# Optimization experiments

Measured on AMD Instinct MI355X. Metric: run time of the kernel, lower is better.

Reference implementation:

```python
import jax, jax.numpy as jnp
import numpy as np

NUM_HEADS = 12


def setup_inputs() -> dict:
    key = jax.random.key(0)
    k1, k2, k3 = jax.random.split(key, 3)
    B, F, P, D = 8, 16, 196, 768
    x = jax.random.normal(k1, (B, F, P, D), dtype=jnp.float32)
    w_qkv = jax.random.normal(k2, (3 * D, D), dtype=jnp.float32) * (D ** -0.5)
    w_proj = jax.random.normal(k3, (D, D), dtype=jnp.float32) * (D ** -0.5)
    b_proj = jnp.zeros((D,), dtype=jnp.float32)
    return {"x": x, "w_qkv": w_qkv, "w_proj": w_proj, "b_proj": b_proj}


def reference(x, w_qkv, w_proj, b_proj):
    B, F, P, D = x.shape
    H = NUM_HEADS
    hd = D // H
    H2 = H // 2
    scale = hd ** -0.5
    N = F * P

    xf = x.reshape(B, N, D)
    qkv = jnp.einsum('bnd,ed->bne', xf, w_qkv)              # (B, N, 3D)
    qkv = qkv.reshape(B, N, 3, H, hd).transpose(2, 0, 3, 1, 4)
    q, k, v = qkv[0], qkv[1], qkv[2]                         # (B, H, N, hd)

    # split heads: first half spatial, second half temporal
    qs, qt = q[:, :H2], q[:, H2:]
    ks, kt = k[:, :H2], k[:, H2:]
    vs, vt = v[:, :H2], v[:, H2:]

    # spatial attention over patches within each frame
    qs = qs.reshape(B * F, H2, P, hd)
    ks = ks.reshape(B * F, H2, P, hd)
    vs = vs.reshape(B * F, H2, P, hd)
    attn_s = jax.nn.softmax(jnp.einsum('nhqd,nhkd->nhqk', qs, ks) * scale, axis=-1)
    ws = jnp.einsum('nhqk,nhkd->nhqd', attn_s, vs)           # (B*F, H2, P, hd)

    # temporal attention: raw row-major reshape, faithful to torch .reshape
    qt = qt.reshape(B * P, H2, F, hd)
    kt = kt.reshape(B * P, H2, F, hd)
    vt = vt.reshape(B * P, H2, F, hd)
    attn_t = jax.nn.softmax(jnp.einsum('mhqd,mhkd->mhqk', qt, kt) * scale, axis=-1)
    wt = jnp.einsum('mhqk,mhkd->mhqd', attn_t, vt)           # (B*P, H2, F, hd)

    ws = ws.reshape(B, H2, N, hd)
    wt = wt.reshape(B, H2, N, hd)
    w = jnp.concatenate([ws, wt], axis=1)                    # (B, H, N, hd)
    w = w.transpose(0, 2, 1, 3).reshape(B, N, D)

    out = jnp.einsum('bnd,ed->bne', w, w_proj) + b_proj
    return out.reshape(B, F, P, D)
```

## Files before the change

### kernel.cpp

```cpp
#include <hip/hip_runtime.h>

#define DEV __device__ __forceinline__

typedef _Float16 half8  __attribute__((ext_vector_type(8)));
typedef _Float16 half4h __attribute__((ext_vector_type(4)));
typedef float    f32x4  __attribute__((ext_vector_type(4)));

static constexpr int Bb = 8;
static constexpr int Ff = 16;
static constexpr int Pp = 196;
static constexpr int Dd = 768;
static constexpr int Hh = 12;
static constexpr int HD = 64;
static constexpr int Nn = 3136;
static constexpr int NC = 392;

#define MFMA(a, b, c) __builtin_amdgcn_mfma_f32_16x16x32_f16(a, b, c, 0, 0, 0)

DEV void gll16(const _Float16* g, _Float16* l) {
  __builtin_amdgcn_global_load_lds(
      (__attribute__((address_space(1))) void*)(g),
      (__attribute__((address_space(3))) void*)(l), 16, 0, 0);
}

DEV void lds_fence() { asm volatile("s_waitcnt lgkmcnt(0)" ::: "memory"); }

__global__ __launch_bounds__(256) void cvt_all(const float* __restrict__ x,
                                               const float* __restrict__ wq,
                                               const float* __restrict__ wp,
                                               _Float16* __restrict__ xh,
                                               _Float16* __restrict__ wqh,
                                               _Float16* __restrict__ wph) {
  const int NX = 4816896, NQ = 442368;
  int i = blockIdx.x * 256 + threadIdx.x;
  const float* s;
  _Float16* d;
  int j;
  if (i < NX) { s = x; d = xh; j = i; }
  else if (i < NX + NQ) { s = wq; d = wqh; j = i - NX; }
  else { s = wp; d = wph; j = i - NX - NQ; }
  f32x4 v = ((const f32x4*)s)[j];
  half4h h;
  h.x = (_Float16)v.x; h.y = (_Float16)v.y;
  h.z = (_Float16)v.z; h.w = (_Float16)v.w;
  ((half4h*)d)[j] = h;
}

__global__ __launch_bounds__(256) void gemm_qkv(const _Float16* __restrict__ X,
                                                const _Float16* __restrict__ W,
                                                _Float16* __restrict__ Q8,
                                                _Float16* __restrict__ K8,
                                                _Float16* __restrict__ V8) {
  __shared__ __align__(16) _Float16 smem[128 * 132];
  _Float16* As = smem;
  _Float16* Bs = smem + 128 * 32;
  const int tid = threadIdx.x;
  const int lane = tid & 63, wid = tid >> 6;
  const int l15 = lane & 15, quad = lane >> 4;
  const int L = blockIdx.x;
  const int v = (L & 7) * 441 + (L >> 3);
  const int bx = v % 18, by = v / 18;
  const int row0 = by * 128;
  const int e0 = bx * 128;
  const int wm = (wid >> 1) * 64, wn = (wid & 1) * 64;

  const _Float16* Ag = X + (size_t)row0 * Dd;
  const _Float16* Bg = W + (size_t)e0 * Dd;

  f32x4 acc[4][4];
#pragma unroll
  for (int i = 0; i < 4; ++i)
#pragma unroll
    for (int j = 0; j < 4; ++j) acc[i][j] = (f32x4)0.0f;

  const int c0 = tid, c1 = tid + 256;
  const int r0s = c0 >> 2, o0 = ((c0 & 3) ^ ((r0s >> 1) & 3)) * 8;
  const int r1s = c1 >> 2, o1 = ((c1 & 3) ^ ((r1s >> 1) & 3)) * 8;
  const int csel = ((quad ^ ((l15 >> 1) & 3))) * 8;

  for (int kt = 0; kt < 24; ++kt) {
    const int k0 = kt * 32;
    __syncthreads();
    gll16(Ag + (size_t)r0s * Dd + k0 + o0, As + c0 * 8);
    gll16(Bg + (size_t)r0s * Dd + k0 + o0, Bs + c0 * 8);
    gll16(Ag + (size_t)r1s * Dd + k0 + o1, As + c1 * 8);
    gll16(Bg + (size_t)r1s * Dd + k0 + o1, Bs + c1 * 8);
    __syncthreads();
    half8 af[4], bf[4];
#pragma unroll
    for (int t = 0; t < 4; ++t) {
      af[t] = *(const half8*)(As + (wm + t * 16 + l15) * 32 + csel);
      bf[t] = *(const half8*)(Bs + (wn + t * 16 + l15) * 32 + csel);
    }
#pragma unroll
    for (int i = 0; i < 4; ++i)
#pragma unroll
      for (int j = 0; j < 4; ++j) acc[i][j] = MFMA(af[i], bf[j], acc[i][j]);
  }

  __syncthreads();
  const int tsel = e0 / Dd;
  if (tsel == 2) {
#pragma unroll
    for (int i = 0; i < 4; ++i)
#pragma unroll
      for (int j = 0; j < 4; ++j) {
        const int m = wm + i * 16 + quad * 4;
        const int n = wn + j * 16 + l15;
        half4h hv;
        hv.x = (_Float16)acc[i][j].x; hv.y = (_Float16)acc[i][j].y;
        hv.z = (_Float16)acc[i][j].z; hv.w = (_Float16)acc[i][j].w;
        *(half4h*)(smem + n * 132 + m) = hv;
      }
    __syncthreads();
    for (int c = tid; c < 2048; c += 256) {
      const int ncl = c >> 7, el = c & 127;
      const int e = e0 + el;
      const int h = (e >> 6) % Hh, d = e & 63;
      const int r = row0 + ncl * 8;
      const int b = r / Nn, n = r % Nn;
      const half4h lo = *(const half4h*)(smem + el * 132 + ncl * 8);
      const half4h hi = *(const half4h*)(smem + el * 132 + ncl * 8 + 4);
      half8 v2;
#pragma unroll
      for (int z = 0; z < 4; ++z) { v2[z] = lo[z]; v2[4 + z] = hi[z]; }
      *(half8*)(V8 + (((size_t)(b * Hh + h) * NC + (n >> 3)) * 64 + d) * 8) = v2;
    }
  } else {
    _Float16* Ob = (tsel == 0) ? Q8 : K8;
#pragma unroll
    for (int i = 0; i < 4; ++i)
#pragma unroll
      for (int j = 0; j < 4; ++j) {
        const int n = wn + j * 16 + l15;
#pragma unroll
        for (int r = 0; r < 4; ++r) {
          const int m = wm + i * 16 + quad * 4 + r;
          smem[m * 132 + n] = (_Float16)acc[i][j][r];
        }
      }
    __syncthreads();
    for (int c = tid; c < 2048; c += 256) {
      const int ec = c >> 7, m = c & 127;
      const int r = row0 + m;
      const int b = r / Nn, n = r % Nn;
      const int e = e0 + ec * 8;
      const int h = (e >> 6) % Hh, dc = (e >> 3) & 7;
      const half4h lo = *(const half4h*)(smem + m * 132 + ec * 8);
      const half4h hi = *(const half4h*)(smem + m * 132 + ec * 8 + 4);
      half8 v2;
#pragma unroll
      for (int z = 0; z < 4; ++z) { v2[z] = lo[z]; v2[4 + z] = hi[z]; }
      *(half8*)(Ob + (((size_t)(b * Hh + h) * 8 + dc) * Nn + n) * 8) = v2;
    }
  }
}

__global__ __launch_bounds__(256) void gemm_proj(const _Float16* __restrict__ Wbuf,
                                                 const _Float16* __restrict__ Wp,
                                                 const float* __restrict__ bias,
                                                 float* __restrict__ Out) {
  __shared__ __align__(16) _Float16 smem[128 * 64];
  _Float16* As = smem;
  _Float16* Bs = smem + 128 * 32;
  const int tid = threadIdx.x;
  const int lane = tid & 63, wid = tid >> 6;
  const int l15 = lane & 15, quad = lane >> 4;
  const int L = blockIdx.x;
  const int v = (L & 7) * 147 + (L >> 3);
  const int bx = v % 6, by = v / 6;
  const int row0 = by * 128;
  const int e0 = bx * 128;
  const int wm = (wid >> 1) * 64, wn = (wid & 1) * 64;

  const _Float16* Ag = Wbuf + (size_t)row0 * Dd;
  const _Float16* Bg = Wp + (size_t)e0 * Dd;

  f32x4 acc[4][4];
#pragma unroll
  for (int i = 0; i < 4; ++i)
#pragma unroll
    for (int j = 0; j < 4; ++j) acc[i][j] = (f32x4)0.0f;

  const int c0 = tid, c1 = tid + 256;
  const int r0s = c0 >> 2, o0 = ((c0 & 3) ^ ((r0s >> 1) & 3)) * 8;
  const int r1s = c1 >> 2, o1 = ((c1 & 3) ^ ((r1s >> 1) & 3)) * 8;
  const int csel = ((quad ^ ((l15 >> 1) & 3))) * 8;

  for (int kt = 0; kt < 24; ++kt) {
    const int k0 = kt * 32;
    __syncthreads();
    gll16(Ag + (size_t)r0s * Dd + k0 + o0, As + c0 * 8);
    gll16(Bg + (size_t)r0s * Dd + k0 + o0, Bs + c0 * 8);
    gll16(Ag + (size_t)r1s * Dd + k0 + o1, As + c1 * 8);
    gll16(Bg + (size_t)r1s * Dd + k0 + o1, Bs + c1 * 8);
    __syncthreads();
    half8 af[4], bf[4];
#pragma unroll
    for (int t = 0; t < 4; ++t) {
      af[t] = *(const half8*)(As + (wm + t * 16 + l15) * 32 + csel);
      bf[t] = *(const half8*)(Bs + (wn + t * 16 + l15) * 32 + csel);
    }
#pragma unroll
    for (int i = 0; i < 4; ++i)
#pragma unroll
      for (int j = 0; j < 4; ++j) acc[i][j] = MFMA(af[i], bf[j], acc[i][j]);
  }

#pragma unroll
  for (int j = 0; j < 4; ++j) {
    const int e = e0 + wn + j * 16 + l15;
    const float bj = bias[e];
#pragma unroll
    for (int i = 0; i < 4; ++i) {
      const int rb = row0 + wm + i * 16 + quad * 4;
#pragma unroll
      for (int r = 0; r < 4; ++r)
        Out[(size_t)(rb + r) * Dd + e] = acc[i][j][r] + bj;
    }
  }
}

__global__ __launch_bounds__(256) void attn_spatial(const _Float16* __restrict__ Q8,
                                                    const _Float16* __restrict__ K8,
                                                    const _Float16* __restrict__ V8,
                                                    _Float16* __restrict__ Wbuf) {
  __shared__ __align__(16) _Float16 Vs[64 * 216];
  __shared__ __align__(16) _Float16 Plds[4][16 * 232];
  const int tid = threadIdx.x;
  const int lane = tid & 63, wid = tid >> 6;
  const int l15 = lane & 15, quad = lane >> 4;
  const int gid = blockIdx.x;
  const int h = gid % 6, f = (gid / 6) % Ff, b = gid / 96;
  const size_t bh = (size_t)b * Hh + h;
  const int g0 = f * Pp;
  const int off = g0 & 7;
  const int nc0 = g0 >> 3;
  const _Float16* Qp = Q8 + bh * 8 * (size_t)Nn * 8;
  const _Float16* Kp = K8 + bh * 8 * (size_t)Nn * 8;

  for (int c = tid; c < 26 * 64; c += 256) {
    const int d = c & 63, ncl = c >> 6;
    const half8 v = *(const half8*)(V8 + ((bh * NC + nc0 + ncl) * 64 + d) * 8);
    _Float16* dst = Vs + d * 216 + (8 - off) + ncl * 8;
    half4h lo, hi;
#pragma unroll
    for (int z = 0; z < 4; ++z) { lo[z] = v[z]; hi[z] = v[4 + z]; }
    *(half4h*)dst = lo;
    *(half4h*)(dst + 4) = hi;
  }
  _Float16* Pw = &Plds[wid][0];
  if (quad < 3) {
    half8 z8;
#pragma unroll
    for (int z = 0; z < 8; ++z) z8[z] = (_Float16)0.0f;
    *(half8*)(Pw + l15 * 232 + 208 + quad * 8) = z8;
  }
  __syncthreads();

  half8 h8z;
#pragma unroll
  for (int z = 0; z < 8; ++z) h8z[z] = (_Float16)0.0f;

  for (int it = 0; it < 4; ++it) {
    const int qi = wid + it * 4;
    if (qi > 12) continue;
    const int qr = qi * 16 + l15;
    const int qtok = g0 + (qr < 195 ? qr : 195);
    const half8 bq0 = *(const half8*)(Qp + ((size_t)quad * Nn + qtok) * 8);
    const half8 bq1 = *(const half8*)(Qp + ((size_t)(quad + 4) * Nn + qtok) * 8);

    f32x4 ex[13];
    float rs = 0.0f;
#pragma unroll
    for (int kt = 0; kt < 13; ++kt) {
      const int krr = kt * 16 + l15;
      const int ktok = g0 + (krr < 195 ? krr : 195);
      const half8 ak0 = *(const half8*)(Kp + ((size_t)quad * Nn + ktok) * 8);
      const half8 ak1 = *(const half8*)(Kp + ((size_t)(quad + 4) * Nn + ktok) * 8);
      f32x4 t = (f32x4)0.0f;
      t = MFMA(ak0, bq0, t);
      t = MFMA(ak1, bq1, t);
      f32x4 e;
#pragma unroll
      for (int r = 0; r < 4; ++r) e[r] = __expf(t[r] * 0.125f);
      if (kt == 12 && quad >= 1) e = (f32x4)0.0f;
      ex[kt] = e;
      rs += e[0] + e[1] + e[2] + e[3];
    }
#pragma unroll
    for (int kt = 0; kt < 13; ++kt)
#pragma unroll
      for (int r = 0; r < 4; ++r)
        Pw[l15 * 232 + kt * 16 + quad * 4 + r] = (_Float16)ex[kt][r];
    rs += __shfl_xor(rs, 16);
    rs += __shfl_xor(rs, 32);
    lds_fence();

    f32x4 acc[4];
#pragma unroll
    for (int mt = 0; mt < 4; ++mt) acc[mt] = (f32x4)0.0f;
#pragma unroll
    for (int c = 0; c < 7; ++c) {
      const half8 bp = *(const half8*)(Pw + l15 * 232 + c * 32 + quad * 8);
      const int k0 = c * 32 + quad * 8;
#pragma unroll
      for (int mt = 0; mt < 4; ++mt) {
        const int d = mt * 16 + l15;
        half8 av = h8z;
        if (k0 < 196) av = *(const half8*)(Vs + d * 216 + 8 + k0);
        acc[mt] = MFMA(av, bp, acc[mt]);
      }
    }
    const float inv = 1.0f / rs;
    if (qr < 196) {
      _Float16* base = Wbuf + (size_t)(b * Nn + g0 + qr) * Dd + h * HD;
#pragma unroll
      for (int mt = 0; mt < 4; ++mt) {
        half4h o;
#pragma unroll
        for (int r = 0; r < 4; ++r) o[r] = (_Float16)(acc[mt][r] * inv);
        *(half4h*)(base + mt * 16 + quad * 4) = o;
      }
    }
    __builtin_amdgcn_sched_barrier(0);
  }
}

__global__ __launch_bounds__(256) void attn_temporal(const _Float16* __restrict__ Q8,
                                                     const _Float16* __restrict__ K8,
                                                     const _Float16* __restrict__ V8,
                                                     _Float16* __restrict__ Wbuf) {
  __shared__ __align__(16) _Float16 Plds[4][16 * 40];
  const int tid = threadIdx.x;
  const int lane = tid & 63, wid = tid >> 6;
  const int l15 = lane & 15, quad = lane >> 4;
  const int p = blockIdx.x * 4 + wid;
  const int J0 = p << 4;
  const int b = J0 / 18816;
  const int rem = J0 % 18816;
  const int hh = rem / Nn;
  const int n0 = rem % Nn;
  const size_t bh = (size_t)b * Hh + 6 + hh;
  const _Float16* Qp = Q8 + bh * 8 * (size_t)Nn * 8;
  const _Float16* Kp = K8 + bh * 8 * (size_t)Nn * 8;
  _Float16* Pw = &Plds[wid][0];

  const int tok = n0 + l15;
  const half8 bq0 = *(const half8*)(Qp + ((size_t)quad * Nn + tok) * 8);
  const half8 bq1 = *(const half8*)(Qp + ((size_t)(quad + 4) * Nn + tok) * 8);
  const half8 ak0 = *(const half8*)(Kp + ((size_t)quad * Nn + tok) * 8);
  const half8 ak1 = *(const half8*)(Kp + ((size_t)(quad + 4) * Nn + tok) * 8);
  f32x4 t = (f32x4)0.0f;
  t = MFMA(ak0, bq0, t);
  t = MFMA(ak1, bq1, t);
  f32x4 e;
#pragma unroll
  for (int r = 0; r < 4; ++r) e[r] = __expf(t[r] * 0.125f);
  float rs = e[0] + e[1] + e[2] + e[3];
  rs += __shfl_xor(rs, 16);
  rs += __shfl_xor(rs, 32);

#pragma unroll
  for (int r = 0; r < 4; ++r) Pw[l15 * 40 + quad * 4 + r] = (_Float16)e[r];
  {
    half4h z4;
    z4.x = z4.y = z4.z = z4.w = (_Float16)0.0f;
    *(half4h*)(Pw + l15 * 40 + 16 + quad * 4) = z4;
  }
  lds_fence();

  const half8 bp = *(const half8*)(Pw + l15 * 40 + quad * 8);
  half8 h8z;
#pragma unroll
  for (int z = 0; z < 8; ++z) h8z[z] = (_Float16)0.0f;

  const float inv = 1.0f / rs;
  _Float16* base = Wbuf + (size_t)(b * Nn + n0 + l15) * Dd + (6 + hh) * HD;
#pragma unroll
  for (int mt = 0; mt < 4; ++mt) {
    const int d = mt * 16 + l15;
    half8 av = h8z;
    if (quad < 2)
      av = *(const half8*)(V8 + ((bh * NC + (n0 >> 3) + quad) * 64 + d) * 8);
    f32x4 acc = (f32x4)0.0f;
    acc = MFMA(av, bp, acc);
    half4h o;
#pragma unroll
    for (int r = 0; r < 4; ++r) o[r] = (_Float16)(acc[r] * inv);
    *(half4h*)(base + mt * 16 + quad * 4) = o;
  }
}

extern "C" void kernel_launch(void* const* d_in, const int* in_sizes, int n_in,
                              void* d_out, int out_size, void* d_ws, size_t ws_size,
                              hipStream_t stream) {
  const float* x = (const float*)d_in[0];
  const float* w_qkv = (const float*)d_in[1];
  const float* w_proj = (const float*)d_in[2];
  const float* b_proj = (const float*)d_in[3];
  float* out = (float*)d_out;

  _Float16* Xh = (_Float16*)d_ws;
  _Float16* Q8 = Xh + 19267584;
  _Float16* K8 = Q8 + 19267584;
  _Float16* V8 = K8 + 19267584;
  _Float16* Wqh = V8 + 19267584;
  _Float16* Wph = Wqh + 1769472;

  cvt_all<<<21120, 256, 0, stream>>>(x, w_qkv, w_proj, Xh, Wqh, Wph);
  gemm_qkv<<<3528, 256, 0, stream>>>(Xh, Wqh, Q8, K8, V8);
  attn_spatial<<<768, 256, 0, stream>>>(Q8, K8, V8, Xh);
  attn_temporal<<<2352, 256, 0, stream>>>(Q8, K8, V8, Xh);
  gemm_proj<<<1176, 256, 0, stream>>>(Xh, Wph, b_proj, out);
}
```

Before: 354.7 us.

## Triple-buffer QKV GEMM LDS tiles with async loads and one barrier per step

The QKV projection GEMM now keeps three LDS stages, issuing async global-to-LDS loads two K-steps ahead. Explicit vmcnt/lgkmcnt waits and a single s_barrier per K-step replace the two __syncthreads around each load, so global latency can overlap the MFMA work. MFMA sections run at raised wave priority, and the launch bounds ask for three blocks per CU. The cost is more LDS per block (48KB) and hand-written wait counts, which would break silently if the number of loads per stage changed.

```diff
diff --git a/kernel.cpp b/kernel.cpp
--- a/kernel.cpp
+++ b/kernel.cpp
@@ -46,14 +46,12 @@
   ((half4h*)d)[j] = h;
 }
 
-__global__ __launch_bounds__(256) void gemm_qkv(const _Float16* __restrict__ X,
-                                                const _Float16* __restrict__ W,
-                                                _Float16* __restrict__ Q8,
-                                                _Float16* __restrict__ K8,
-                                                _Float16* __restrict__ V8) {
-  __shared__ __align__(16) _Float16 smem[128 * 132];
-  _Float16* As = smem;
-  _Float16* Bs = smem + 128 * 32;
+__global__ __launch_bounds__(256, 3) void gemm_qkv(const _Float16* __restrict__ X,
+                                                   const _Float16* __restrict__ W,
+                                                   _Float16* __restrict__ Q8,
+                                                   _Float16* __restrict__ K8,
+                                                   _Float16* __restrict__ V8) {
+  __shared__ __align__(16) _Float16 smem[3 * 8192];
   const int tid = threadIdx.x;
   const int lane = tid & 63, wid = tid >> 6;
   const int l15 = lane & 15, quad = lane >> 4;
@@ -78,24 +76,47 @@
   const int r1s = c1 >> 2, o1 = ((c1 & 3) ^ ((r1s >> 1) & 3)) * 8;
   const int csel = ((quad ^ ((l15 >> 1) & 3))) * 8;
 
-  for (int kt = 0; kt < 24; ++kt) {
-    const int k0 = kt * 32;
-    __syncthreads();
-    gll16(Ag + (size_t)r0s * Dd + k0 + o0, As + c0 * 8);
-    gll16(Bg + (size_t)r0s * Dd + k0 + o0, Bs + c0 * 8);
-    gll16(Ag + (size_t)r1s * Dd + k0 + o1, As + c1 * 8);
-    gll16(Bg + (size_t)r1s * Dd + k0 + o1, Bs + c1 * 8);
-    __syncthreads();
+  auto stage = [&](int t) {
+    const int kn = t * 32;
+    _Float16* An = smem + (t % 3) * 8192;
+    _Float16* Bn = An + 4096;
+    gll16(Ag + (size_t)r0s * Dd + kn + o0, An + c0 * 8);
+    gll16(Bg + (size_t)r0s * Dd + kn + o0, Bn + c0 * 8);
+    gll16(Ag + (size_t)r1s * Dd + kn + o1, An + c1 * 8);
+    gll16(Bg + (size_t)r1s * Dd + kn + o1, Bn + c1 * 8);
+  };
+
+  stage(0);
+  stage(1);
+  asm volatile("s_waitcnt vmcnt(4)" ::: "memory");
+  asm volatile("s_barrier" ::: "memory");
+
+  auto tile = [&](int T, int SL, bool STG, bool WLAST) {
+    if (STG) stage(T + 2);
+    const _Float16* As_ = smem + SL * 8192;
+    const _Float16* Bs_ = As_ + 4096;
     half8 af[4], bf[4];
 #pragma unroll
-    for (int t = 0; t < 4; ++t) {
-      af[t] = *(const half8*)(As + (wm + t * 16 + l15) * 32 + csel);
-      bf[t] = *(const half8*)(Bs + (wn + t * 16 + l15) * 32 + csel);
-    }
+    for (int x = 0; x < 4; ++x) {
+      af[x] = *(const half8*)(As_ + (wm + x * 16 + l15) * 32 + csel);
+      bf[x] = *(const half8*)(Bs_ + (wn + x * 16 + l15) * 32 + csel);
+    }
+    if (WLAST) asm volatile("s_waitcnt vmcnt(0) lgkmcnt(0)" ::: "memory");
+    else       asm volatile("s_waitcnt vmcnt(4) lgkmcnt(0)" ::: "memory");
+    asm volatile("s_barrier" ::: "memory");
+    __builtin_amdgcn_s_setprio(1);
 #pragma unroll
     for (int i = 0; i < 4; ++i)
 #pragma unroll
       for (int j = 0; j < 4; ++j) acc[i][j] = MFMA(af[i], bf[j], acc[i][j]);
+    __builtin_amdgcn_s_setprio(0);
+  };
+
+#pragma unroll
+  for (int g = 0; g < 8; ++g) {
+    tile(3 * g,     0, true,    false);
+    tile(3 * g + 1, 1, (g < 7), (g == 7));
+    tile(3 * g + 2, 2, (g < 7), (g == 7));
   }
 
   __syncthreads();
```

Result: no change. 358.0 us (+0.9%).
